# Optimization experiments

Measured on AMD Instinct MI355X. Metric: run time of the kernel, lower is better.

The kernel has to match this reference:

```python
import jax, jax.numpy as jnp
import numpy as np

M, N, K, D_IN = 200, 6, 25, 784
GAMMA, EPS = 0.5, 0.5
TOTAL = M * N


def setup_inputs() -> dict:
    key = jax.random.key(0)
    ks = jax.random.split(key, 8)
    B = 16384
    def lin(kk, shape, fan_in):
        bound = 1.0 / np.sqrt(fan_in)
        return jax.random.uniform(kk, shape, jnp.float32, -bound, bound)
    return {
        "batch_x": jax.random.normal(ks[0], (B, D_IN), jnp.float32),
        "Wa": lin(ks[1], (M, D_IN), D_IN),
        "ba": lin(ks[2], (M,), D_IN),
        "Wb": lin(ks[3], (TOTAL, TOTAL), TOTAL),
        "bb": lin(ks[4], (TOTAL,), TOTAL),
        "Wd": lin(ks[5], (D_IN, M), M),
        "bd": lin(ks[6], (D_IN,), M),
    }


def _step(params, carry, x):
    Wa, ba, Wb, bb, Wd, bd = params
    x_b, phi, psi = carry
    # sigma: per-group drive broadcast over cells + full recurrent term, shape (m, n)
    z_a = (Wa @ x + ba)[:, None]                      # (m, 1)
    z_b = (Wb @ x_b + bb).reshape(M, N)               # (m, n)
    sigma = z_a + z_b
    # inhibited activity
    pi = (1.0 - phi) * (sigma - sigma.min() + 1.0)    # (m, n)
    lambda_i = pi.max(axis=1)                         # (m,)
    # top-1 cell per group (scatter of topk indices == one-hot argmax)
    M_pi = jax.nn.one_hot(jnp.argmax(pi, axis=1), N, dtype=sigma.dtype)
    # top-k groups
    _, idx = jax.lax.top_k(lambda_i, K)
    M_lambda = jnp.zeros((M,), sigma.dtype).at[idx].set(1.0)[:, None]
    y = jnp.tanh(M_pi * M_lambda * sigma)             # (m, n)
    x_a_pred = Wd @ y.max(axis=1) + bd                # (D_in,)
    # memory / inhibition updates
    psi_n = jnp.maximum(EPS * psi, y)
    phi_n = jnp.maximum(GAMMA * phi, y)
    alpha = psi_n.sum()
    alpha = jnp.where(alpha == 0.0, 1.0, alpha)
    x_b_n = (psi_n / alpha).reshape(-1)
    # original detaches the recurrent state each step
    carry_n = (jax.lax.stop_gradient(x_b_n),
               jax.lax.stop_gradient(phi_n),
               jax.lax.stop_gradient(psi_n))
    return carry_n, x_a_pred


def reference(batch_x, Wa, ba, Wb, bb, Wd, bd):
    params = (Wa, ba, Wb, bb, Wd, bd)
    carry0 = (jnp.zeros((TOTAL,), batch_x.dtype),
              jnp.zeros((M, N), batch_x.dtype),
              jnp.zeros((M, N), batch_x.dtype))
    (x_b, phi, psi), preds = jax.lax.scan(
        lambda c, x: _step(params, c, x), carry0, batch_x)
    return preds, x_b, phi, psi
```

## Files before the change

kernel.cpp:

```cpp
#include <hip/hip_runtime.h>
#include <math.h>

#define Tn   16384
#define Mg   200
#define Nc   6
#define TOT  1200
#define Kk   25
#define Din  784

__global__ void transpose_k(const float* __restrict__ src, float* __restrict__ dst,
                            int R, int C) {
    __shared__ float tile[32][33];
    int bx = blockIdx.x * 32, by = blockIdx.y * 32;
    int x = bx + threadIdx.x;
    for (int j = 0; j < 32; j += 8) {
        int y = by + threadIdx.y + j;
        if (x < C && y < R) tile[threadIdx.y + j][threadIdx.x] = src[(size_t)y * C + x];
    }
    __syncthreads();
    int x2 = by + threadIdx.x;
    for (int j = 0; j < 32; j += 8) {
        int y2 = bx + threadIdx.y + j;
        if (x2 < R && y2 < C) dst[(size_t)y2 * R + x2] = tile[threadIdx.x][threadIdx.y + j];
    }
}

__global__ void za_k(const float* __restrict__ X, const float* __restrict__ Wa,
                     const float* __restrict__ ba, float* __restrict__ Za) {
    __shared__ float xs[16][788];
    const int tid = threadIdx.x;
    const int t0  = blockIdx.x * 16;
    for (int idx = tid; idx < 16 * Din; idx += 256) {
        int tt = idx / Din, kk = idx - tt * Din;
        xs[tt][kk] = X[(size_t)(t0 + tt) * Din + kk];
    }
    __syncthreads();
    const int tq = tid & 15, gq = tid >> 4;
    const float4* xrow = reinterpret_cast<const float4*>(&xs[tq][0]);
    for (int g = gq; g < Mg; g += 16) {
        float acc = ba[g];
        const float4* wrow = reinterpret_cast<const float4*>(Wa + (size_t)g * Din);
        for (int k4 = 0; k4 < Din / 4; ++k4) {
            float4 a = xrow[k4], b = wrow[k4];
            acc = fmaf(a.x, b.x, acc); acc = fmaf(a.y, b.y, acc);
            acc = fmaf(a.z, b.z, acc); acc = fmaf(a.w, b.w, acc);
        }
        Za[(size_t)(t0 + tq) * Mg + g] = acc;
    }
}

__launch_bounds__(384, 1)
__global__ void serial_k(const float* __restrict__ Za, const float* __restrict__ WbT,
                         const float* __restrict__ bb,
                         unsigned long long* __restrict__ YP,
                         float* __restrict__ outTail) {
    __shared__ alignas(16) float u_sh[TOT];
    __shared__ alignas(16) unsigned long long sel[26];

    const int tid = threadIdx.x;

    if (tid < TOT / 4)
        *reinterpret_cast<float4*>(u_sh + 4 * tid) = make_float4(0.f, 0.f, 0.f, 0.f);
    if (tid == 383) sel[25] = 0ull;
    __syncthreads();

    if (tid < 64) {
        const int lane = tid;
        const bool grp = (lane < 50);
        const int cell0 = 24 * lane;
        const unsigned long long lt = (1ull << lane) - 1ull;

        float u[24], ps[24], cb[24];
        #pragma unroll
        for (int i = 0; i < 24; ++i) { u[i] = 0.f; ps[i] = 0.f; cb[i] = 0.f; }
        if (grp) {
            #pragma unroll
            for (int q = 0; q < 6; ++q) {
                float4 v = *reinterpret_cast<const float4*>(bb + cell0 + 4 * q);
                cb[4*q] = v.x; cb[4*q+1] = v.y; cb[4*q+2] = v.z; cb[4*q+3] = v.w;
            }
        }
        float alpha = 0.f;
        float4 za4 = make_float4(0.f, 0.f, 0.f, 0.f);
        if (grp) za4 = *reinterpret_cast<const float4*>(Za + 4 * lane);

        for (int t = 0; t < Tn; ++t) {
            float4 zan = make_float4(0.f, 0.f, 0.f, 0.f);
            if (grp && t + 1 < Tn)
                zan = *reinterpret_cast<const float4*>(Za + (size_t)(t + 1) * Mg + 4 * lane);

            if (grp) {
                #pragma unroll
                for (int q = 0; q < 6; ++q) {
                    float4 v = *reinterpret_cast<const float4*>(u_sh + cell0 + 4 * q);
                    u[4*q] = v.x; u[4*q+1] = v.y; u[4*q+2] = v.z; u[4*q+3] = v.w;
                }
            }
            const float inv = (alpha == 0.f) ? 1.f : (1.f / alpha);

            float lm = INFINITY;
            if (grp) {
                #pragma unroll
                for (int c = 0; c < 4; ++c) {
                    float zc = (c==0)?za4.x:(c==1)?za4.y:(c==2)?za4.z:za4.w;
                    #pragma unroll
                    for (int j = 0; j < 6; ++j) {
                        int i = 6 * c + j;
                        u[i] = fmaf(u[i], inv, cb[i] + zc);
                        lm = fminf(lm, u[i]);
                    }
                }
            }
            #pragma unroll
            for (int o = 1; o < 64; o <<= 1) lm = fminf(lm, __shfl_xor(lm, o));
            const float m1 = 1.f - lm;

            float bs[4], bp[4]; int bj[4]; unsigned long long kb[4];
            #pragma unroll
            for (int c = 0; c < 4; ++c) { bs[c]=0.f; bp[c]=0.f; bj[c]=0; kb[c]=0ull; }
            if (grp) {
                #pragma unroll
                for (int c = 0; c < 4; ++c) {
                    float best = -INFINITY, sbv = 0.f, pbv = 0.f; int jb = 0;
                    #pragma unroll
                    for (int j = 0; j < 6; ++j) {
                        int i = 6 * c + j;
                        float pv = (1.f - ps[i]) * (u[i] + m1);
                        bool bet = pv > best;
                        best = bet ? pv : best;
                        jb  = bet ? j : jb;
                        sbv = bet ? u[i] : sbv;
                        pbv = bet ? ps[i] : pbv;
                    }
                    unsigned ub = __float_as_uint(best);
                    ub ^= (unsigned)(((int)ub) >> 31) | 0x80000000u;
                    int g = 4 * lane + c;
                    kb[c] = ((unsigned long long)ub << 32) |
                            (unsigned long long)(0xFFFFFFFFu - (unsigned)g);
                    bs[c] = sbv; bp[c] = pbv; bj[c] = jb;
                }
            }

            unsigned long long A = 0ull, B = ~0ull;
            unsigned long long p = __shfl(kb[0], 0);
            unsigned long long theta;
            while (true) {
                int cnt = __popcll(__ballot(kb[0] >= p)) + __popcll(__ballot(kb[1] >= p))
                        + __popcll(__ballot(kb[2] >= p)) + __popcll(__ballot(kb[3] >= p));
                if (cnt == Kk) { theta = p; break; }
                if (cnt > Kk) A = p; else B = p;
                unsigned long long m0 = __ballot(kb[0] > A && kb[0] < B);
                unsigned long long m1b = __ballot(kb[1] > A && kb[1] < B);
                unsigned long long m2 = __ballot(kb[2] > A && kb[2] < B);
                unsigned long long m3 = __ballot(kb[3] > A && kb[3] < B);
                int cls; unsigned long long mm;
                if (m0)       { cls = 0; mm = m0; }
                else if (m1b) { cls = 1; mm = m1b; }
                else if (m2)  { cls = 2; mm = m2; }
                else          { cls = 3; mm = m3; }
                int sl = __ffsll(mm) - 1;
                unsigned long long kc = (cls==0)?kb[0]:(cls==1)?kb[1]:(cls==2)?kb[2]:kb[3];
                p = __shfl(kc, sl);
            }

            unsigned long long M0 = __ballot(kb[0] >= theta);
            unsigned long long M1 = __ballot(kb[1] >= theta);
            unsigned long long M2 = __ballot(kb[2] >= theta);
            unsigned long long M3 = __ballot(kb[3] >= theta);
            int base1 = __popcll(M0);
            int base2 = base1 + __popcll(M1);
            int base3 = base2 + __popcll(M2);

            float dsum = 0.f;
            #pragma unroll
            for (int c = 0; c < 4; ++c) {
                unsigned long long Mc = (c==0)?M0:(c==1)?M1:(c==2)?M2:M3;
                int bse = (c==0)?0:(c==1)?base1:(c==2)?base2:base3;
                bool s = grp && (kb[c] >= theta);
                float d = 0.f;
                if (s) {
                    int slot = bse + __popcll(Mc & lt);
                    float x = fminf(fmaxf(bs[c], -9.f), 9.f);
                    float e = __expf(2.f * x);
                    float y = 1.f - 2.f / (e + 1.f);
                    float yv = fmaxf(y, 0.f);
                    d = fmaxf(y - 0.5f * bp[c], 0.f);
                    int g = 4 * lane + c;
                    int eix = 6 * g + bj[c];
                    sel[slot] = ((unsigned long long)(unsigned)(eix * TOT) << 32) |
                                (unsigned long long)__float_as_uint(d);
                    YP[(size_t)t * Kk + slot] =
                        ((unsigned long long)(unsigned)g << 32) |
                        (unsigned long long)__float_as_uint(yv);
                }
                dsum += d;
                #pragma unroll
                for (int j = 0; j < 6; ++j) {
                    int i = 6 * c + j;
                    float add = (j == bj[c]) ? d : 0.f;
                    ps[i] = fmaf(ps[i], 0.5f, add);
                }
            }
            #pragma unroll
            for (int o = 1; o < 64; o <<= 1) dsum += __shfl_xor(dsum, o);
            alpha = fmaf(alpha, 0.5f, dsum);

            __syncthreads();
            __syncthreads();
            za4 = zan;
        }

        if (grp) {
            float inv2 = (alpha == 0.f) ? 1.f : (1.f / alpha);
            #pragma unroll
            for (int i = 0; i < 24; ++i) {
                outTail[cell0 + i]           = ps[i] * inv2;
                outTail[TOT + cell0 + i]     = ps[i];
                outTail[2 * TOT + cell0 + i] = ps[i];
            }
        }
    } else {
        const int j = tid - 64;
        const bool act = (j < 300);
        float* up = u_sh + 4 * j;

        for (int t = 0; t < Tn; ++t) {
            float4 uo = make_float4(0.f, 0.f, 0.f, 0.f);
            if (act) {
                uo = *reinterpret_cast<const float4*>(up);
                uo.x *= 0.5f; uo.y *= 0.5f; uo.z *= 0.5f; uo.w *= 0.5f;
            }
            __syncthreads();

            ulonglong2 sr[13];
            const ulonglong2* S = reinterpret_cast<const ulonglong2*>(sel);
            #pragma unroll
            for (int q = 0; q < 13; ++q) sr[q] = S[q];
            float sd[Kk]; int so[Kk];
            #pragma unroll
            for (int k = 0; k < Kk; ++k) {
                unsigned long long v = (k & 1) ? sr[k >> 1].y : sr[k >> 1].x;
                sd[k] = __uint_as_float((unsigned)v);
                so[k] = (int)(v >> 32);
            }
            if (act) {
                float4 c[Kk];
                #pragma unroll
                for (int k = 0; k < Kk; ++k)
                    c[k] = *reinterpret_cast<const float4*>(WbT + so[k] + 4 * j);
                __builtin_amdgcn_sched_barrier(0);
                #pragma unroll
                for (int k = 0; k < Kk; ++k) {
                    float dk = sd[k];
                    uo.x = fmaf(dk, c[k].x, uo.x);
                    uo.y = fmaf(dk, c[k].y, uo.y);
                    uo.z = fmaf(dk, c[k].z, uo.z);
                    uo.w = fmaf(dk, c[k].w, uo.w);
                }
                *reinterpret_cast<float4*>(up) = uo;
            }
            __syncthreads();
        }
    }
}

__global__ void preds_k(const unsigned long long* __restrict__ YP,
                        const float* __restrict__ WdT, const float* __restrict__ bd,
                        float* __restrict__ out) {
    const int t = blockIdx.x;
    __shared__ float sv[Kk];
    __shared__ int   si[Kk];
    if (threadIdx.x < Kk) {
        unsigned long long v = YP[(size_t)t * Kk + threadIdx.x];
        sv[threadIdx.x] = __uint_as_float((unsigned)v);
        si[threadIdx.x] = (int)(v >> 32);
    }
    __syncthreads();
    for (int d = threadIdx.x; d < Din; d += 256) {
        float acc = bd[d];
        #pragma unroll
        for (int k = 0; k < Kk; ++k)
            acc = fmaf(sv[k], WdT[(size_t)si[k] * Din + d], acc);
        out[(size_t)t * Din + d] = acc;
    }
}

extern "C" void kernel_launch(void* const* d_in, const int* in_sizes, int n_in,
                              void* d_out, int out_size, void* d_ws, size_t ws_size,
                              hipStream_t stream) {
    const float* X  = (const float*)d_in[0];
    const float* Wa = (const float*)d_in[1];
    const float* ba = (const float*)d_in[2];
    const float* Wb = (const float*)d_in[3];
    const float* bb = (const float*)d_in[4];
    const float* Wd = (const float*)d_in[5];
    const float* bd = (const float*)d_in[6];
    float* out = (float*)d_out;

    float* w    = (float*)d_ws;
    float* Za   = w;
    float* WbT  = Za  + (size_t)Tn * Mg;
    float* WdT  = WbT + (size_t)TOT * TOT;
    unsigned long long* YP =
        (unsigned long long*)(WdT + (size_t)Mg * Din);

    dim3 tb(32, 8);
    transpose_k<<<dim3((TOT + 31) / 32, (TOT + 31) / 32), tb, 0, stream>>>(Wb, WbT, TOT, TOT);
    transpose_k<<<dim3((Mg + 31) / 32, (Din + 31) / 32), tb, 0, stream>>>(Wd, WdT, Din, Mg);
    za_k<<<Tn / 16, 256, 0, stream>>>(X, Wa, ba, Za);
    serial_k<<<1, 384, 0, stream>>>(Za, WbT, bb, YP, out + (size_t)Tn * Din);
    preds_k<<<Tn, 256, 0, stream>>>(YP, WdT, bd, out);
}
```

Before: 75.39 ms.

## Move sigma assembly and global min into worker waves of serial kernel

```diff
diff --git a/kernel.cpp b/kernel.cpp
--- a/kernel.cpp
+++ b/kernel.cpp
@@ -7,6 +7,7 @@
 #define TOT  1200
 #define Kk   25
 #define Din  784
+#define SP   28
 
 __global__ void transpose_k(const float* __restrict__ src, float* __restrict__ dst,
                             int R, int C) {
@@ -54,66 +55,44 @@
                          const float* __restrict__ bb,
                          unsigned long long* __restrict__ YP,
                          float* __restrict__ outTail) {
-    __shared__ alignas(16) float u_sh[TOT];
-    __shared__ alignas(16) unsigned long long sel[26];
-
-    const int tid = threadIdx.x;
-
-    if (tid < TOT / 4)
-        *reinterpret_cast<float4*>(u_sh + 4 * tid) = make_float4(0.f, 0.f, 0.f, 0.f);
-    if (tid == 383) sel[25] = 0ull;
-    __syncthreads();
+    __shared__ alignas(16) float sigma_sh[50 * SP];
+    __shared__ alignas(16) float minp[8];
+    __shared__ alignas(16) float selD[32];
+    __shared__ alignas(16) int   selO[32];
+    __shared__ float alphaS;
+
+    const int tid  = threadIdx.x;
+    const int lane = tid & 63;
 
     if (tid < 64) {
-        const int lane = tid;
         const bool grp = (lane < 50);
+        const int sgb  = lane * SP;
         const int cell0 = 24 * lane;
         const unsigned long long lt = (1ull << lane) - 1ull;
 
-        float u[24], ps[24], cb[24];
+        float ps[24];
         #pragma unroll
-        for (int i = 0; i < 24; ++i) { u[i] = 0.f; ps[i] = 0.f; cb[i] = 0.f; }
-        if (grp) {
-            #pragma unroll
-            for (int q = 0; q < 6; ++q) {
-                float4 v = *reinterpret_cast<const float4*>(bb + cell0 + 4 * q);
-                cb[4*q] = v.x; cb[4*q+1] = v.y; cb[4*q+2] = v.z; cb[4*q+3] = v.w;
-            }
-        }
+        for (int i = 0; i < 24; ++i) ps[i] = 0.f;
         float alpha = 0.f;
-        float4 za4 = make_float4(0.f, 0.f, 0.f, 0.f);
-        if (grp) za4 = *reinterpret_cast<const float4*>(Za + 4 * lane);
+
+        __syncthreads();
 
         for (int t = 0; t < Tn; ++t) {
-            float4 zan = make_float4(0.f, 0.f, 0.f, 0.f);
-            if (grp && t + 1 < Tn)
-                zan = *reinterpret_cast<const float4*>(Za + (size_t)(t + 1) * Mg + 4 * lane);
-
+            float4 mp4 = *reinterpret_cast<const float4*>(minp);
+            float m = fminf(fminf(fminf(mp4.x, mp4.y), fminf(mp4.z, mp4.w)), minp[4]);
+            const float m1 = 1.f - m;
+
+            float sg[24];
             if (grp) {
                 #pragma unroll
                 for (int q = 0; q < 6; ++q) {
-                    float4 v = *reinterpret_cast<const float4*>(u_sh + cell0 + 4 * q);
-                    u[4*q] = v.x; u[4*q+1] = v.y; u[4*q+2] = v.z; u[4*q+3] = v.w;
+                    float4 v = *reinterpret_cast<const float4*>(sigma_sh + sgb + 4 * q);
+                    sg[4*q] = v.x; sg[4*q+1] = v.y; sg[4*q+2] = v.z; sg[4*q+3] = v.w;
                 }
-            }
-            const float inv = (alpha == 0.f) ? 1.f : (1.f / alpha);
-
-            float lm = INFINITY;
-            if (grp) {
+            } else {
                 #pragma unroll
-                for (int c = 0; c < 4; ++c) {
-                    float zc = (c==0)?za4.x:(c==1)?za4.y:(c==2)?za4.z:za4.w;
-                    #pragma unroll
-                    for (int j = 0; j < 6; ++j) {
-                        int i = 6 * c + j;
-                        u[i] = fmaf(u[i], inv, cb[i] + zc);
-                        lm = fminf(lm, u[i]);
-                    }
-                }
-            }
-            #pragma unroll
-            for (int o = 1; o < 64; o <<= 1) lm = fminf(lm, __shfl_xor(lm, o));
-            const float m1 = 1.f - lm;
+                for (int i = 0; i < 24; ++i) sg[i] = 0.f;
+            }
 
             float bs[4], bp[4]; int bj[4]; unsigned long long kb[4];
             #pragma unroll
@@ -125,11 +104,11 @@
                     #pragma unroll
                     for (int j = 0; j < 6; ++j) {
                         int i = 6 * c + j;
-                        float pv = (1.f - ps[i]) * (u[i] + m1);
+                        float pv = (1.f - ps[i]) * (sg[i] + m1);
                         bool bet = pv > best;
                         best = bet ? pv : best;
                         jb  = bet ? j : jb;
-                        sbv = bet ? u[i] : sbv;
+                        sbv = bet ? sg[i] : sbv;
                         pbv = bet ? ps[i] : pbv;
                     }
                     unsigned ub = __float_as_uint(best);
@@ -172,8 +151,10 @@
             int base3 = base2 + __popcll(M2);
 
             float dsum = 0.f;
+            int slotr[4]; unsigned long long yv64[4];
             #pragma unroll
             for (int c = 0; c < 4; ++c) {
+                slotr[c] = -1; yv64[c] = 0ull;
                 unsigned long long Mc = (c==0)?M0:(c==1)?M1:(c==2)?M2:M3;
                 int bse = (c==0)?0:(c==1)?base1:(c==2)?base2:base3;
                 bool s = grp && (kb[c] >= theta);
@@ -186,12 +167,11 @@
                     float yv = fmaxf(y, 0.f);
                     d = fmaxf(y - 0.5f * bp[c], 0.f);
                     int g = 4 * lane + c;
-                    int eix = 6 * g + bj[c];
-                    sel[slot] = ((unsigned long long)(unsigned)(eix * TOT) << 32) |
-                                (unsigned long long)__float_as_uint(d);
-                    YP[(size_t)t * Kk + slot] =
-                        ((unsigned long long)(unsigned)g << 32) |
-                        (unsigned long long)__float_as_uint(yv);
+                    selD[slot] = d;
+                    selO[slot] = (6 * g + bj[c]) * TOT;
+                    slotr[c] = slot;
+                    yv64[c] = ((unsigned long long)(unsigned)g << 32) |
+                              (unsigned long long)__float_as_uint(yv);
                 }
                 dsum += d;
                 #pragma unroll
@@ -204,10 +184,13 @@
             #pragma unroll
             for (int o = 1; o < 64; o <<= 1) dsum += __shfl_xor(dsum, o);
             alpha = fmaf(alpha, 0.5f, dsum);
+            if (lane == 0) alphaS = (alpha == 0.f) ? 1.f : alpha;
 
             __syncthreads();
+            #pragma unroll
+            for (int c = 0; c < 4; ++c)
+                if (slotr[c] >= 0) YP[(size_t)t * Kk + slotr[c]] = yv64[c];
             __syncthreads();
-            za4 = zan;
         }
 
         if (grp) {
@@ -222,43 +205,75 @@
     } else {
         const int j = tid - 64;
         const bool act = (j < 300);
-        float* up = u_sh + 4 * j;
+        const int w = (tid >> 6) - 1;
+        const int base = act ? 4 * j : 0;
+        const int saddr = act ? ((j / 6) * SP + (4 * j) % 24) : 0;
+        const int g0 = base / 6, g1 = (base + 3) / 6;
+        const bool f1 = ((base + 1) / 6) != g0;
+        const bool f2 = ((base + 2) / 6) != g0;
+        const bool f3 = ((base + 3) / 6) != g0;
+
+        float4 cb4 = make_float4(0.f, 0.f, 0.f, 0.f);
+        if (act) cb4 = *reinterpret_cast<const float4*>(bb + base);
+        float za0 = act ? Za[g0] : 0.f;
+        float za1 = act ? Za[g1] : 0.f;
+        float4 uo = make_float4(0.f, 0.f, 0.f, 0.f);
+
+        {
+            float s0 = cb4.x + za0;
+            float s1 = cb4.y + (f1 ? za1 : za0);
+            float s2 = cb4.z + (f2 ? za1 : za0);
+            float s3 = cb4.w + (f3 ? za1 : za0);
+            if (act)
+                *reinterpret_cast<float4*>(sigma_sh + saddr) = make_float4(s0,s1,s2,s3);
+            float lm = act ? fminf(fminf(s0, s1), fminf(s2, s3)) : INFINITY;
+            #pragma unroll
+            for (int o = 1; o < 64; o <<= 1) lm = fminf(lm, __shfl_xor(lm, o));
+            if (lane == 0) minp[w] = lm;
+        }
+        __syncthreads();
 
         for (int t = 0; t < Tn; ++t) {
-            float4 uo = make_float4(0.f, 0.f, 0.f, 0.f);
-            if (act) {
-                uo = *reinterpret_cast<const float4*>(up);
-                uo.x *= 0.5f; uo.y *= 0.5f; uo.z *= 0.5f; uo.w *= 0.5f;
-            }
+            const int tn = (t + 1 < Tn) ? t + 1 : t;
+            float nza0 = act ? Za[(size_t)tn * Mg + g0] : 0.f;
+            float nza1 = act ? Za[(size_t)tn * Mg + g1] : 0.f;
+            uo.x *= 0.5f; uo.y *= 0.5f; uo.z *= 0.5f; uo.w *= 0.5f;
+
             __syncthreads();
 
-            ulonglong2 sr[13];
-            const ulonglong2* S = reinterpret_cast<const ulonglong2*>(sel);
-            #pragma unroll
-            for (int q = 0; q < 13; ++q) sr[q] = S[q];
-            float sd[Kk]; int so[Kk];
+            float vD = 0.f; int vO = 0;
+            if (lane < 25) { vD = selD[lane]; vO = selO[lane]; }
+            const float av  = alphaS;
+            const float inv = 1.f / av;
+
+            float4 cc[Kk];
             #pragma unroll
             for (int k = 0; k < Kk; ++k) {
-                unsigned long long v = (k & 1) ? sr[k >> 1].y : sr[k >> 1].x;
-                sd[k] = __uint_as_float((unsigned)v);
-                so[k] = (int)(v >> 32);
-            }
-            if (act) {
-                float4 c[Kk];
-                #pragma unroll
-                for (int k = 0; k < Kk; ++k)
-                    c[k] = *reinterpret_cast<const float4*>(WbT + so[k] + 4 * j);
-                __builtin_amdgcn_sched_barrier(0);
-                #pragma unroll
-                for (int k = 0; k < Kk; ++k) {
-                    float dk = sd[k];
-                    uo.x = fmaf(dk, c[k].x, uo.x);
-                    uo.y = fmaf(dk, c[k].y, uo.y);
-                    uo.z = fmaf(dk, c[k].z, uo.z);
-                    uo.w = fmaf(dk, c[k].w, uo.w);
-                }
-                *reinterpret_cast<float4*>(up) = uo;
-            }
+                int offk = __builtin_amdgcn_readlane(vO, k);
+                cc[k] = *reinterpret_cast<const float4*>(WbT + offk + base);
+            }
+            __builtin_amdgcn_sched_barrier(0);
+            #pragma unroll
+            for (int k = 0; k < Kk; ++k) {
+                float dk = __uint_as_float(
+                    (unsigned)__builtin_amdgcn_readlane((int)__float_as_uint(vD), k));
+                uo.x = fmaf(dk, cc[k].x, uo.x);
+                uo.y = fmaf(dk, cc[k].y, uo.y);
+                uo.z = fmaf(dk, cc[k].z, uo.z);
+                uo.w = fmaf(dk, cc[k].w, uo.w);
+            }
+
+            float s0 = fmaf(uo.x, inv, cb4.x + nza0);
+            float s1 = fmaf(uo.y, inv, cb4.y + (f1 ? nza1 : nza0));
+            float s2 = fmaf(uo.z, inv, cb4.z + (f2 ? nza1 : nza0));
+            float s3 = fmaf(uo.w, inv, cb4.w + (f3 ? nza1 : nza0));
+            if (act)
+                *reinterpret_cast<float4*>(sigma_sh + saddr) = make_float4(s0,s1,s2,s3);
+            float lm = act ? fminf(fminf(s0, s1), fminf(s2, s3)) : INFINITY;
+            #pragma unroll
+            for (int o = 1; o < 64; o <<= 1) lm = fminf(lm, __shfl_xor(lm, o));
+            if (lane == 0) minp[w] = lm;
+
             __syncthreads();
         }
     }
```

New measurement: 72.82 ms. -3.4%, faster.
